# Optimization experiments

Measured on AMD Instinct MI355X. Metric: run time of the kernel, lower is better.

Reference implementation:

```python
import jax, jax.numpy as jnp
import numpy as np
from functools import partial

EPS = 1e-6
SINKHORN_ITERS = 10

def sinkhorn(logits):
    # log-space Sinkhorn normalization -> doubly-stochastic soft permutation
    M = logits
    for _ in range(SINKHORN_ITERS):
        M = M - jax.scipy.special.logsumexp(M, axis=1, keepdims=True)
        M = M - jax.scipy.special.logsumexp(M, axis=0, keepdims=True)
    return jnp.exp(M)

def r_poly(a):
    delta = 0.5 - a
    num = 0.25 + 1.65811 * delta + 2.15388 * delta**2 + 8.2844 * delta**3 + 6.16764 * delta**4
    den = a * (1.0 - a)
    den = jnp.where(jnp.abs(den) < EPS, EPS, den)
    return num / den

def power_r(x, y, ra, w0, w1):
    ra = jnp.where(jnp.abs(ra) < EPS, EPS, ra)
    return (w0 * x**ra + w1 * y**ra) ** (1.0 / ra)

def F_upper(x, y, a, w0, w1):
    # generalized combine for a in [0.5, 2); x,y pre-clamped to [EPS, 1-EPS]
    xy = x * y
    mn = jnp.minimum(x, y)
    lin = w0 * x + w1 * y
    p = jnp.sqrt(jnp.maximum(3.0 / jnp.maximum(2.0 - a, EPS) - 1.0, EPS))
    r1 = xy ** p                                      # 1.25 < a < 2
    r3 = 4.0 * ((1.25 - a) * mn + (a - 1.0) * xy)     # 1 < a < 1.25
    ra = r_poly(jnp.clip(a, 0.75, 1.0 - EPS))
    r5 = power_r(x, y, ra, w0, w1)                    # 0.75 <= a < 1
    R = r_poly(jnp.float32(0.75))
    r6 = (3.0 - 4.0 * a) * lin + (4.0 * a - 2.0) * power_r(x, y, R, w0, w1)
    r0 = jnp.where((jnp.abs(x - 1.0) < EPS) & (jnp.abs(y - 1.0) < EPS), 1.0, 0.0)
    out = lin                                          # a ~ 0.5 / fallback
    out = jnp.where((a > 0.5) & (a < 0.75), r6, out)
    out = jnp.where((a >= 0.75) & (a < 1.0), r5, out)
    out = jnp.where(jnp.abs(a - 1.0) < EPS, mn, out)
    out = jnp.where((a > 1.0) & (a < 1.25), r3, out)
    out = jnp.where(jnp.abs(a - 1.25) < EPS, xy, out)
    out = jnp.where((a > 1.25) & (a < 2.0), r1, out)
    out = jnp.where(jnp.abs(a - 2.0) < EPS, r0, out)
    return out

def F_comb(x, y, a, w0, w1):
    x = jnp.clip(jnp.nan_to_num(x, nan=EPS), EPS, 1.0 - EPS)
    y = jnp.clip(jnp.nan_to_num(y, nan=EPS), EPS, 1.0 - EPS)
    a = jnp.clip(jnp.nan_to_num(a, nan=-1.0, posinf=2.0 - EPS, neginf=-1.0 + EPS), -1.0 + EPS, 2.0 - EPS)
    hi = F_upper(x, y, a, w0, w1)
    a_flip = jnp.clip(1.0 - a, -1.0 + EPS, 2.0 - EPS)
    lo = 1.0 - F_upper(1.0 - x, 1.0 - y, a_flip, w0, w1)  # rule 8 (single-level recursion)
    return jnp.where(a < 0.5 - EPS, lo, hi)

def combine(left, right, w, b):
    w_soft = jax.nn.softmax(w)
    a_scaled = jax.nn.sigmoid(b) * 3.0 - 1.0
    nres = F_comb(left, right, a_scaled, w_soft[0], w_soft[1])
    return jnp.where(jnp.isnan(nres), a_scaled, nres)

def setup_inputs() -> dict:
    key = jax.random.key(0)
    k1, k2, k3, k4 = jax.random.split(key, 4)
    B, L = 65536, 256
    x = jax.random.uniform(k1, (B, L), dtype=jnp.float32)
    logits = jax.random.normal(k2, (L, L), dtype=jnp.float32)
    weights = jax.random.uniform(k3, (L - 1, 2), dtype=jnp.float32) + 0.5   # uniform(0.5, 1.5)
    biases = jax.random.uniform(k4, (L - 1,), dtype=jnp.float32) * 3.0 - 1.0
    return {"x": x, "logits": logits, "weights": weights, "biases": biases}

def reference(x, logits, weights, biases):
    P = sinkhorn(logits)                  # (L, L) soft permutation
    leaf_values = x @ P                   # (B, L)
    leaves = leaf_values.T                # (L, B)
    out0 = combine(leaves[0], leaves[1], weights[0], biases[0])

    def step(carry, inp):
        leaf, w, b = inp
        out = combine(carry, leaf, w, b)
        return out, None

    final, _ = jax.lax.scan(step, out0, (leaves[2:], weights[1:], biases[1:]))
    return final[:, None]                 # (B, 1)
```

## Files before the change

kernel.cpp:

```cpp
#include <hip/hip_runtime.h>

#define EPS 1e-6f

typedef unsigned short u16;
typedef u16   u16x4  __attribute__((ext_vector_type(4)));
typedef u16   u16x8  __attribute__((ext_vector_type(8)));
typedef float f32x4  __attribute__((ext_vector_type(4)));
typedef _Float16 f16x8 __attribute__((ext_vector_type(8)));

enum { BR_LIN = 0, BR_R6, BR_R5, BR_MIN, BR_R3, BR_XY, BR_R1, BR_R0 };

__device__ __forceinline__ u16 f2h(float f) { return __builtin_bit_cast(u16, (_Float16)f); }

__device__ __forceinline__ f16x8 lds_f16x8(const u16* p) {
  u16x8 r = *(const u16x8*)p;
  return __builtin_bit_cast(f16x8, r);
}

__device__ __forceinline__ f32x4 mfma16(f16x8 a, f16x8 b, f32x4 c) {
  return __builtin_amdgcn_mfma_f32_16x16x32_f16(a, b, c, 0, 0, 0);
}

__device__ __forceinline__ float fexp2(float x) {
  float r; asm("v_exp_f32 %0, %1" : "=v"(r) : "v"(x)); return r;
}
__device__ __forceinline__ float flog2(float x) {
  float r; asm("v_log_f32 %0, %1" : "=v"(r) : "v"(x)); return r;
}

__device__ __forceinline__ float r_poly_f(float a) {
  float d  = 0.5f - a;
  float d2 = d * d;
  float num = 0.25f + 1.65811f * d + 2.15388f * d2 + 8.2844f * d2 * d + 6.16764f * d2 * d2;
  float den = a * (1.0f - a);
  if (fabsf(den) < EPS) den = EPS;
  return num / den;
}

__device__ __forceinline__ float step2(float carry, float leaf,
                                       f32x4 p0, f32x4 p1, f32x4 p2) {
  float fx = p0[0], w0 = p0[1], w1 = p0[2], s_lin = p0[3];
  float s_mn = p1[0], s_xy = p1[1], s_pm = p1[2], s_pow = p1[3];
  float rs = p2[0], rinv = p2[1], cp = p2[2], sx = p2[3];

  float xx = fminf(fmaxf(carry, EPS), 1.0f - EPS);
  float yy = fminf(fmaxf(leaf,  EPS), 1.0f - EPS);
  float X = fmaf(sx, xx, fx);
  float Y = fmaf(sx, yy, fx);

  float lx = flog2(X), ly = flog2(Y);
  float pw = fexp2(cp * (lx + ly));
  float ex = fexp2(rs * lx), ey = fexp2(rs * ly);
  float s  = fmaf(w0, ex, w1 * ey);
  float pm = fexp2(rinv * flog2(s));

  float r = s_lin * fmaf(w0, X, w1 * Y);
  r = fmaf(s_mn, fminf(X, Y), r);
  r = fmaf(s_xy, X * Y, r);
  r = fmaf(s_pm, pm, r);
  r = fmaf(s_pow, pw, r);
  return fmaf(sx, r, fx);
}

__global__ void param_kernel(const float* __restrict__ W, const float* __restrict__ Bv,
                             float* __restrict__ prm12, int n) {
  int i = blockIdx.x * blockDim.x + threadIdx.x;
  if (i >= n) return;
  float w0r = W[2 * i], w1r = W[2 * i + 1];
  float m  = fmaxf(w0r, w1r);
  float e0 = expf(w0r - m), e1 = expf(w1r - m);
  float inv = 1.0f / (e0 + e1);
  float w0 = e0 * inv, w1 = e1 * inv;

  float b   = Bv[i];
  float sig = 1.0f / (1.0f + expf(-b));
  float a_fb = sig * 3.0f - 1.0f;

  float a = a_fb;
  if (__builtin_isnan(a)) a = -1.0f;
  a = fminf(fmaxf(a, -1.0f + EPS), 2.0f - EPS);
  int flip = (a < 0.5f - EPS) ? 1 : 0;
  float aa = a;
  if (flip) aa = fminf(fmaxf(1.0f - a, -1.0f + EPS), 2.0f - EPS);

  int br; float c0 = 0.f, c1 = 0.f, c2 = 0.f, c3 = 0.f;
  if (fabsf(aa - 2.0f) < EPS) br = BR_R0;
  else if (aa > 1.25f && aa < 2.0f) {
    br = BR_R1;
    c0 = sqrtf(fmaxf(3.0f / fmaxf(2.0f - aa, EPS) - 1.0f, EPS));
  } else if (fabsf(aa - 1.25f) < EPS) br = BR_XY;
  else if (aa > 1.0f && aa < 1.25f) { br = BR_R3; c0 = 1.25f - aa; c1 = aa - 1.0f; }
  else if (fabsf(aa - 1.0f) < EPS) br = BR_MIN;
  else if (aa >= 0.75f && aa < 1.0f) {
    br = BR_R5;
    float ac = fminf(fmaxf(aa, 0.75f), 1.0f - EPS);
    float ra = r_poly_f(ac);
    if (fabsf(ra) < EPS) ra = EPS;
    c0 = ra; c1 = 1.0f / ra;
  } else if (aa > 0.5f && aa < 0.75f) {
    br = BR_R6;
    c0 = 3.0f - 4.0f * aa; c1 = 4.0f * aa - 2.0f;
    float R = r_poly_f(0.75f);
    if (fabsf(R) < EPS) R = EPS;
    c2 = R; c3 = 1.0f / R;
  } else br = BR_LIN;

  float s_lin = 0.f, s_mn = 0.f, s_xy = 0.f, s_pm = 0.f, s_pow = 0.f;
  float rs = 1.0f, rinv = 1.0f, cp = 0.0f;
  if (br == BR_R1)       { s_pow = 1.0f; cp = c0; }
  else if (br == BR_XY)  { s_xy = 1.0f; }
  else if (br == BR_R3)  { s_mn = 4.0f * c0; s_xy = 4.0f * c1; }
  else if (br == BR_MIN) { s_mn = 1.0f; }
  else if (br == BR_R5)  { s_pm = 1.0f; rs = c0; rinv = c1; }
  else if (br == BR_R6)  { s_lin = c0; s_pm = c1; rs = c2; rinv = c3; }
  else if (br == BR_LIN) { s_lin = 1.0f; }

  float* o12 = prm12 + i * 12;
  o12[0] = (float)flip; o12[1] = w0;  o12[2] = w1;   o12[3] = s_lin;
  o12[4] = s_mn;        o12[5] = s_xy; o12[6] = s_pm; o12[7] = s_pow;
  o12[8] = rs;          o12[9] = rinv; o12[10] = cp;  o12[11] = 1.0f - 2.0f * (float)flip;
}

__global__ __launch_bounds__(1024, 4) void sinkhorn_kernel(
    const float* __restrict__ logits, u16* __restrict__ PTf) {
  __shared__ float alpha[256], beta[256];
  __shared__ float psum[256][33];

  const int t  = threadIdx.x;
  const int R  = t >> 5;
  const int C  = t & 31;
  const int r0 = R << 3;

  float e[8][8];
  #pragma unroll
  for (int dr = 0; dr < 8; ++dr) {
    const float* row = logits + (r0 + dr) * 256 + C;
    #pragma unroll
    for (int m = 0; m < 8; ++m) e[dr][m] = __expf(row[m << 5]);
  }

  if (t < 256) beta[t] = 1.0f;
  __syncthreads();

  for (int it = 0; it < 10; ++it) {
    {
      float bv[8], acc[8];
      #pragma unroll
      for (int m = 0; m < 8; ++m) bv[m] = beta[C + (m << 5)];
      #pragma unroll
      for (int dr = 0; dr < 8; ++dr) {
        float s = 0.f;
        #pragma unroll
        for (int m = 0; m < 8; ++m) s += e[dr][m] * bv[m];
        acc[dr] = s;
      }
      #pragma unroll
      for (int dr = 0; dr < 8; ++dr) psum[r0 + dr][C] = acc[dr];
    }
    __syncthreads();
    if (t < 256) {
      float s = 0.f;
      #pragma unroll
      for (int j = 0; j < 32; ++j) s += psum[t][j];
      alpha[t] = 1.0f / s;
    }
    __syncthreads();
    {
      float av[8], acc[8];
      #pragma unroll
      for (int dr = 0; dr < 8; ++dr) av[dr] = alpha[r0 + dr];
      #pragma unroll
      for (int m = 0; m < 8; ++m) {
        float s = 0.f;
        #pragma unroll
        for (int dr = 0; dr < 8; ++dr) s += e[dr][m] * av[dr];
        acc[m] = s;
      }
      #pragma unroll
      for (int m = 0; m < 8; ++m) psum[C + (m << 5)][R] = acc[m];
    }
    __syncthreads();
    if (t < 256) {
      float s = 0.f;
      #pragma unroll
      for (int j = 0; j < 32; ++j) s += psum[t][j];
      beta[t] = 1.0f / s;
    }
    __syncthreads();
  }

  float av[8], bv[8];
  #pragma unroll
  for (int dr = 0; dr < 8; ++dr) av[dr] = alpha[r0 + dr];
  #pragma unroll
  for (int m = 0; m < 8; ++m) bv[m] = beta[C + (m << 5)];

  #pragma unroll
  for (int m = 0; m < 8; ++m) {
    int l = C + (m << 5);
    u16x8 vh;
    #pragma unroll
    for (int dr = 0; dr < 8; ++dr) vh[dr] = f2h(av[dr] * e[dr][m] * bv[m]);
    *(u16x8*)(PTf + l * 256 + r0) = vh;
  }
}

#define CSTR 132

__global__ __launch_bounds__(512, 4) void gemm_chain_kernel(
    const float* __restrict__ x, const u16* __restrict__ PTf,
    const float* __restrict__ prm12, float* __restrict__ out) {
  __shared__ __align__(16) char smem[46080];
  u16* xs = (u16*)smem;
  u16* pt = (u16*)(smem + 8192);
  float* cbuf = (float*)smem;
  float* qlds = (float*)(smem + 33792);

  const int t    = threadIdx.x;
  const int w    = t >> 6;
  const int lane = t & 63;
  const int bl   = lane & 15;
  const int kh   = lane >> 4;
  const int wm   = w >> 2;
  const int wn   = w & 3;
  const int b0   = blockIdx.x * 128;

  const int xrow = t >> 3;
  const int xc4  = t & 7;

  for (int j = t; j < 3060; j += 512) qlds[j] = prm12[j];

  f32x4 acc[8][2];
  #pragma unroll
  for (int m = 0; m < 8; ++m) {
    acc[m][0] = f32x4{0.f, 0.f, 0.f, 0.f};
    acc[m][1] = f32x4{0.f, 0.f, 0.f, 0.f};
  }

  f32x4 xr[2];
  u16x8 pr[2];

  #pragma unroll
  for (int j = 0; j < 2; ++j) {
    xr[j] = *(const f32x4*)(x + (b0 + xrow + 64 * j) * 256 + (xc4 << 2));
    int c = t + 512 * j, r = c >> 2, s = c & 3, g = s ^ ((r >> 1) & 3);
    pr[j] = *(const u16x8*)(PTf + r * 256 + (g << 3));
  }

  for (int kc = 0; kc < 8; ++kc) {
    #pragma unroll
    for (int j = 0; j < 2; ++j) {
      int row = xrow + 64 * j;
      u16x4 hv;
      #pragma unroll
      for (int e = 0; e < 4; ++e) hv[e] = f2h(xr[j][e]);
      int g = xc4 >> 1, sub = xc4 & 1;
      *(u16x4*)(xs + row * 32 + ((g ^ ((row >> 1) & 3)) << 3) + (sub << 2)) = hv;
      *(u16x8*)(pt + ((t + 512 * j) << 3)) = pr[j];
    }
    __syncthreads();

    if (kc < 7) {
      int k1 = (kc + 1) << 5;
      #pragma unroll
      for (int j = 0; j < 2; ++j) {
        xr[j] = *(const f32x4*)(x + (b0 + xrow + 64 * j) * 256 + k1 + (xc4 << 2));
        int c = t + 512 * j, r = c >> 2, s = c & 3, g = s ^ ((r >> 1) & 3);
        pr[j] = *(const u16x8*)(PTf + r * 256 + k1 + (g << 3));
      }
    }

    f16x8 bh[2];
    #pragma unroll
    for (int nf = 0; nf < 2; ++nf) {
      int brow = (wn << 5) + (nf << 4) + bl;
      bh[nf] = lds_f16x8(xs + brow * 32 + ((kh ^ ((brow >> 1) & 3)) << 3));
    }
    #pragma unroll
    for (int mf = 0; mf < 8; ++mf) {
      int arow = (wm << 7) + (mf << 4) + bl;
      f16x8 ah = lds_f16x8(pt + arow * 32 + ((kh ^ ((arow >> 1) & 3)) << 3));
      #pragma unroll
      for (int nf = 0; nf < 2; ++nf)
        acc[mf][nf] = mfma16(ah, bh[nf], acc[mf][nf]);
    }
    __syncthreads();
  }

  float carry = 0.0f;

  #pragma unroll
  for (int c = 0; c < 4; ++c) {
    __syncthreads();
    if (wm == (c >> 1)) {
      #pragma unroll
      for (int d = 0; d < 4; ++d) {
        int mf = ((c & 1) << 2) + d;
        #pragma unroll
        for (int nf = 0; nf < 2; ++nf) {
          int bc = (wn << 5) + (nf << 4) + bl;
          #pragma unroll
          for (int r = 0; r < 4; ++r) {
            int lr = (d << 4) + (kh << 2) + r;
            cbuf[lr * CSTR + bc] = acc[mf][nf][r];
          }
        }
      }
    }
    __syncthreads();
    if (t < 128) {
      int lc0 = 0;
      if (c == 0) {
        float v0 = cbuf[0 * CSTR + t];
        float v1 = cbuf[1 * CSTR + t];
        float v2 = cbuf[2 * CSTR + t];
        float v3 = cbuf[3 * CSTR + t];
        carry = v0;
        carry = step2(carry, v1, *(const f32x4*)(qlds),      *(const f32x4*)(qlds + 4),  *(const f32x4*)(qlds + 8));
        carry = step2(carry, v2, *(const f32x4*)(qlds + 12), *(const f32x4*)(qlds + 16), *(const f32x4*)(qlds + 20));
        carry = step2(carry, v3, *(const f32x4*)(qlds + 24), *(const f32x4*)(qlds + 28), *(const f32x4*)(qlds + 32));
        lc0 = 4;
      }
      for (int lc = lc0; lc < 64; lc += 4) {
        float v[4];
        #pragma unroll
        for (int u = 0; u < 4; ++u) v[u] = cbuf[(lc + u) * CSTR + t];
        #pragma unroll
        for (int u = 0; u < 4; ++u) {
          int node = (c << 6) + lc + u - 1;
          const float* qn = qlds + node * 12;
          carry = step2(carry, v[u],
                        *(const f32x4*)(qn), *(const f32x4*)(qn + 4), *(const f32x4*)(qn + 8));
        }
      }
    }
  }
  if (t < 128) out[b0 + t] = carry;
}

extern "C" void kernel_launch(void* const* d_in, const int* in_sizes, int n_in,
                              void* d_out, int out_size, void* d_ws, size_t ws_size,
                              hipStream_t stream) {
  const float* x       = (const float*)d_in[0];
  const float* logits  = (const float*)d_in[1];
  const float* weights = (const float*)d_in[2];
  const float* biases  = (const float*)d_in[3];
  float* out = (float*)d_out;

  char* ws = (char*)d_ws;
  int Btot = in_sizes[0] / 256;

  u16*   PTf   = (u16*)ws;
  float* prm12 = (float*)(ws + 131072);

  param_kernel<<<1, 256, 0, stream>>>(weights, biases, prm12, 255);
  sinkhorn_kernel<<<1, 1024, 0, stream>>>(logits, PTf);
  gemm_chain_kernel<<<Btot / 128, 512, 0, stream>>>(x, PTf, prm12, out);
}
```

Baseline: 83.09 us.

## Shuffle-reduce Sinkhorn row sums and hoist leaf-only math off carry chain

In the Sinkhorn kernel, the row-sum reduction now uses wave shuffles over the 32 column lanes instead of an LDS round trip. This removes two barriers and one serial reduction phase per iteration. In the sequential combine chain, work that depends only on the leaf (log, exp, weight products) is split out and computed ahead for four leaves. That shortens the carry-dependent critical path, at the cost of more live registers.

```diff
diff --git a/kernel.cpp b/kernel.cpp
--- a/kernel.cpp
+++ b/kernel.cpp
@@ -37,24 +37,32 @@
   return num / den;
 }
 
-__device__ __forceinline__ float step2(float carry, float leaf,
-                                       f32x4 p0, f32x4 p1, f32x4 p2) {
-  float fx = p0[0], w0 = p0[1], w1 = p0[2], s_lin = p0[3];
+__device__ __forceinline__ void leaf_pre(float leaf, f32x4 p0, f32x4 p2,
+                                         float& Y, float& w1Y, float& w1ey, float& cply) {
+  float fx = p0[0], w1 = p0[2], rs = p2[0], cp = p2[2], sx = p2[3];
+  float yy = fminf(fmaxf(leaf, EPS), 1.0f - EPS);
+  Y = fmaf(sx, yy, fx);
+  float ly = flog2(Y);
+  w1Y  = w1 * Y;
+  w1ey = w1 * fexp2(rs * ly);
+  cply = cp * ly;
+}
+
+__device__ __forceinline__ float step_carry(float carry, float Y, float w1Y, float w1ey, float cply,
+                                            f32x4 p0, f32x4 p1, f32x4 p2) {
+  float fx = p0[0], w0 = p0[1], s_lin = p0[3];
   float s_mn = p1[0], s_xy = p1[1], s_pm = p1[2], s_pow = p1[3];
   float rs = p2[0], rinv = p2[1], cp = p2[2], sx = p2[3];
 
   float xx = fminf(fmaxf(carry, EPS), 1.0f - EPS);
-  float yy = fminf(fmaxf(leaf,  EPS), 1.0f - EPS);
-  float X = fmaf(sx, xx, fx);
-  float Y = fmaf(sx, yy, fx);
-
-  float lx = flog2(X), ly = flog2(Y);
-  float pw = fexp2(cp * (lx + ly));
-  float ex = fexp2(rs * lx), ey = fexp2(rs * ly);
-  float s  = fmaf(w0, ex, w1 * ey);
+  float X  = fmaf(sx, xx, fx);
+  float lx = flog2(X);
+  float pw = fexp2(fmaf(cp, lx, cply));
+  float ex = fexp2(rs * lx);
+  float s  = fmaf(w0, ex, w1ey);
   float pm = fexp2(rinv * flog2(s));
 
-  float r = s_lin * fmaf(w0, X, w1 * Y);
+  float r = s_lin * fmaf(w0, X, w1Y);
   r = fmaf(s_mn, fminf(X, Y), r);
   r = fmaf(s_xy, X * Y, r);
   r = fmaf(s_pm, pm, r);
@@ -123,7 +131,7 @@
 
 __global__ __launch_bounds__(1024, 4) void sinkhorn_kernel(
     const float* __restrict__ logits, u16* __restrict__ PTf) {
-  __shared__ float alpha[256], beta[256];
+  __shared__ float beta[256];
   __shared__ float psum[256][33];
 
   const int t  = threadIdx.x;
@@ -142,9 +150,11 @@
   if (t < 256) beta[t] = 1.0f;
   __syncthreads();
 
+  float ar[8];
+
   for (int it = 0; it < 10; ++it) {
     {
-      float bv[8], acc[8];
+      float bv[8];
       #pragma unroll
       for (int m = 0; m < 8; ++m) bv[m] = beta[C + (m << 5)];
       #pragma unroll
@@ -152,46 +162,39 @@
         float s = 0.f;
         #pragma unroll
         for (int m = 0; m < 8; ++m) s += e[dr][m] * bv[m];
-        acc[dr] = s;
-      }
-      #pragma unroll
-      for (int dr = 0; dr < 8; ++dr) psum[r0 + dr][C] = acc[dr];
+        ar[dr] = s;
+      }
+      #pragma unroll
+      for (int dr = 0; dr < 8; ++dr) {
+        float s = ar[dr];
+        s += __shfl_xor(s, 1);
+        s += __shfl_xor(s, 2);
+        s += __shfl_xor(s, 4);
+        s += __shfl_xor(s, 8);
+        s += __shfl_xor(s, 16);
+        ar[dr] = 1.0f / s;
+      }
+    }
+    {
+      #pragma unroll
+      for (int m = 0; m < 8; ++m) {
+        float s = 0.f;
+        #pragma unroll
+        for (int dr = 0; dr < 8; ++dr) s += e[dr][m] * ar[dr];
+        psum[C + (m << 5)][R] = s;
+      }
     }
     __syncthreads();
     if (t < 256) {
       float s = 0.f;
       #pragma unroll
       for (int j = 0; j < 32; ++j) s += psum[t][j];
-      alpha[t] = 1.0f / s;
-    }
-    __syncthreads();
-    {
-      float av[8], acc[8];
-      #pragma unroll
-      for (int dr = 0; dr < 8; ++dr) av[dr] = alpha[r0 + dr];
-      #pragma unroll
-      for (int m = 0; m < 8; ++m) {
-        float s = 0.f;
-        #pragma unroll
-        for (int dr = 0; dr < 8; ++dr) s += e[dr][m] * av[dr];
-        acc[m] = s;
-      }
-      #pragma unroll
-      for (int m = 0; m < 8; ++m) psum[C + (m << 5)][R] = acc[m];
-    }
-    __syncthreads();
-    if (t < 256) {
-      float s = 0.f;
-      #pragma unroll
-      for (int j = 0; j < 32; ++j) s += psum[t][j];
       beta[t] = 1.0f / s;
     }
     __syncthreads();
   }
 
-  float av[8], bv[8];
-  #pragma unroll
-  for (int dr = 0; dr < 8; ++dr) av[dr] = alpha[r0 + dr];
+  float bv[8];
   #pragma unroll
   for (int m = 0; m < 8; ++m) bv[m] = beta[C + (m << 5)];
 
@@ -200,7 +203,7 @@
     int l = C + (m << 5);
     u16x8 vh;
     #pragma unroll
-    for (int dr = 0; dr < 8; ++dr) vh[dr] = f2h(av[dr] * e[dr][m] * bv[m]);
+    for (int dr = 0; dr < 8; ++dr) vh[dr] = f2h(ar[dr] * e[dr][m] * bv[m]);
     *(u16x8*)(PTf + l * 256 + r0) = vh;
   }
 }
@@ -316,22 +319,36 @@
         float v2 = cbuf[2 * CSTR + t];
         float v3 = cbuf[3 * CSTR + t];
         carry = v0;
-        carry = step2(carry, v1, *(const f32x4*)(qlds),      *(const f32x4*)(qlds + 4),  *(const f32x4*)(qlds + 8));
-        carry = step2(carry, v2, *(const f32x4*)(qlds + 12), *(const f32x4*)(qlds + 16), *(const f32x4*)(qlds + 20));
-        carry = step2(carry, v3, *(const f32x4*)(qlds + 24), *(const f32x4*)(qlds + 28), *(const f32x4*)(qlds + 32));
+        float vv[3] = {v1, v2, v3};
+        #pragma unroll
+        for (int u = 0; u < 3; ++u) {
+          const float* qn = qlds + u * 12;
+          f32x4 P0 = *(const f32x4*)(qn), P1 = *(const f32x4*)(qn + 4), P2 = *(const f32x4*)(qn + 8);
+          float Y, w1Y, w1ey, cply;
+          leaf_pre(vv[u], P0, P2, Y, w1Y, w1ey, cply);
+          carry = step_carry(carry, Y, w1Y, w1ey, cply, P0, P1, P2);
+        }
         lc0 = 4;
       }
       for (int lc = lc0; lc < 64; lc += 4) {
         float v[4];
         #pragma unroll
         for (int u = 0; u < 4; ++u) v[u] = cbuf[(lc + u) * CSTR + t];
+        f32x4 P0[4], P1[4], P2[4];
         #pragma unroll
         for (int u = 0; u < 4; ++u) {
-          int node = (c << 6) + lc + u - 1;
-          const float* qn = qlds + node * 12;
-          carry = step2(carry, v[u],
-                        *(const f32x4*)(qn), *(const f32x4*)(qn + 4), *(const f32x4*)(qn + 8));
+          const float* qn = qlds + ((c << 6) + lc + u - 1) * 12;
+          P0[u] = *(const f32x4*)(qn);
+          P1[u] = *(const f32x4*)(qn + 4);
+          P2[u] = *(const f32x4*)(qn + 8);
         }
+        float Y[4], w1Y[4], w1ey[4], cply[4];
+        #pragma unroll
+        for (int u = 0; u < 4; ++u)
+          leaf_pre(v[u], P0[u], P2[u], Y[u], w1Y[u], w1ey[u], cply[u]);
+        #pragma unroll
+        for (int u = 0; u < 4; ++u)
+          carry = step_carry(carry, Y[u], w1Y[u], w1ey[u], cply[u], P0[u], P1[u], P2[u]);
       }
     }
   }
```

Result: slower. 112.4 us (+35.3%).
